# Kernel optimization log

Measured on AMD Instinct MI355X. Metric: run time of the kernel, lower is better.

## Reference

```python
import jax, jax.numpy as jnp
from jax import lax
import numpy as np

T = 131072  # trajectory length


def _model_matrices():
    # F: constant-velocity model on augmented state [pose_t; pose_{t-1}]
    I6 = jnp.eye(6, dtype=jnp.float32)
    F = jnp.zeros((12, 12), dtype=jnp.float32)
    F = F.at[:6, :6].set(2.0 * I6)
    F = F.at[:6, 6:].set(-I6)
    F = F.at[6:, :6].set(I6)
    G = jnp.zeros((12, 6), dtype=jnp.float32)
    G = G.at[:6, :6].set(I6)
    return F, G


def setup_inputs() -> dict:
    key = jax.random.key(0)
    k1, = jax.random.split(key, 1)
    pose_measurements = jax.random.normal(k1, (T, 6), dtype=jnp.float32)
    # SPD noise covariances (scaled identities, as typical in the repo's config)
    process_noise_cov = 0.01 * jnp.eye(6, dtype=jnp.float32)
    measure_noise_cov = 0.05 * jnp.eye(6, dtype=jnp.float32)
    cov_init = jnp.eye(12, dtype=jnp.float32)  # _covariance_matrix_pred buffer
    return {
        "pose_measurements": pose_measurements,
        "process_noise_cov": process_noise_cov,
        "measure_noise_cov": measure_noise_cov,
        "cov_init": cov_init,
    }


def reference(pose_measurements, process_noise_cov, measure_noise_cov, cov_init):
    F, G = _model_matrices()
    Q_aug = G @ process_noise_cov @ G.T  # [[Q, 0], [0, 0]]  (12,12)
    I12 = jnp.eye(12, dtype=jnp.float32)
    z6 = jnp.zeros((12, 6), dtype=jnp.float32)

    def step(carry, meas):
        est, P = carry  # est: (12,), P: (12,12)
        # _predict
        v = est[:6] - est[6:]
        pred = jnp.concatenate([est[:6] + v, est[:6]])  # (12,)
        Pp = F @ P @ F.T + Q_aug
        # _update
        S = Pp[:6, :6] + measure_noise_cov            # (6,6)
        K = Pp[:, :6] @ jnp.linalg.inv(S)             # (12,6)
        est_new = pred + K @ (meas - pred[:6])        # (12,)
        KH = jnp.concatenate([K, z6], axis=1)         # (12,12)
        P_new = (I12 - KH) @ Pp
        return (est_new, P_new), (pred, est_new)

    # rows 0,1 initialized from measurements
    row0 = jnp.concatenate([pose_measurements[0], jnp.zeros(6, dtype=jnp.float32)])
    row1 = jnp.concatenate([pose_measurements[1], pose_measurements[0]])

    (_, _), (preds, ests) = lax.scan(step, (row1, cov_init), pose_measurements[2:])

    head = jnp.stack([row0, row1])                   # (2,12)
    pose_estimate = jnp.concatenate([head, ests], axis=0)    # (T,12)
    pose_prediction = jnp.concatenate([head, preds], axis=0)  # (T,12)
    velocity_estimate = pose_estimate[1:-1, :6] - pose_estimate[1:-1, 6:]

    return (pose_estimate[:, :6], pose_prediction[:, :6], velocity_estimate)
```

## Files before the change

### kernel.cpp

```cpp
#include <hip/hip_runtime.h>

#define T_LEN   131072
#define NSTEPS  (T_LEN - 2)
#define CHUNK   16
#define NCHUNK  8192
#define NCJ     (NCHUNK * 6)
#define CAP     512
#define CPB     64
#define NBLK    (NCHUNK / CPB)
#define K2T     (CPB * 6)

#define OFF_STEADY 16
#define OFF_K1     32
#define OFF_K2     (OFF_K1 + CAP * 4)
#define OFF_LP     (OFF_K2 + CAP * 4)
#define OFF_BT     (OFF_LP + NCHUNK * 16 * 4)
#define OFF_BI     (OFF_BT + NBLK * 16 * 4)

__device__ __forceinline__ int riccati(const float* pnc, const float* mnc,
                                       const float* cov, float* g1t, float* g2t,
                                       float& k1o, float& k2o) {
    float q = pnc[0], r = mnc[0];
    float a = cov[0], b = cov[6], c = cov[6 * 12 + 6];
    float pk1 = -1e30f, pk2 = -1e30f, k1 = 0.f, k2 = 0.f;
    int stable = 0, s;
    for (s = 0; s < CAP; ++s) {
        float bp = 2.0f * a - b;
        float t2 = 2.0f * b - c;
        float ap = 2.0f * bp - t2 + q;
        float cp = a;
        float S  = ap + r;
        float invS = 1.0f / S;
        k1 = ap * invS;
        k2 = bp * invS;
        g1t[s] = k1;
        g2t[s] = k2;
        float om = 1.0f - k1;
        a = om * ap;
        b = om * bp;
        c = cp - k2 * bp;
        if (fabsf(k1 - pk1) <= 5e-7f * fabsf(k1) &&
            fabsf(k2 - pk2) <= 5e-7f * (fabsf(k2) + 1e-20f)) {
            if (++stable >= 8) { ++s; break; }
        } else {
            stable = 0;
        }
        pk1 = k1; pk2 = k2;
    }
    k1o = k1; k2o = k2;
    return s;
}

__global__ __launch_bounds__(K2T) void k_chunk_scan(
    const float* __restrict__ meas, const float* __restrict__ pnc,
    const float* __restrict__ mnc, const float* __restrict__ cov,
    float* __restrict__ ws_f, int* __restrict__ ws_i,
    float* __restrict__ lp, float* __restrict__ btot) {
    __shared__ float g1t[CAP], g2t[CAP];
    __shared__ float lm[CPB][5];
    __shared__ float lu[CPB][13];
    __shared__ int   s_sc;
    __shared__ float s_k1, s_k2;
    int tid = threadIdx.x;
    int cl = tid / 6;
    int j  = tid - 6 * cl;
    int b  = blockIdx.x;
    if (tid == 0) {
        float k1, k2;
        int sc = riccati(pnc, mnc, cov, g1t, g2t, k1, k2);
        s_sc = sc; s_k1 = k1; s_k2 = k2;
    }
    __syncthreads();
    int sc = s_sc;
    float k1s = s_k1, k2s = s_k2;
    if (b == 0) {
        for (int t = tid; t < sc; t += K2T) {
            ws_f[OFF_K1 / 4 + t] = g1t[t];
            ws_f[OFF_K2 / 4 + t] = g2t[t];
        }
        if (tid == 0) {
            ws_i[0] = sc;
            ws_f[OFF_STEADY / 4]     = k1s;
            ws_f[OFF_STEADY / 4 + 1] = k2s;
        }
    }
    int c = b * CPB + cl;
    int s0 = c * CHUNK;
    float m00 = 1.f, m01 = 0.f, m10 = 0.f, m11 = 1.f;
    float u0 = 0.f, u1 = 0.f;
#pragma unroll
    for (int i = 0; i < CHUNK; ++i) {
        int s = s0 + i;
        if (s < NSTEPS) {
            float g1, g2;
            if (b == 0) {
                int si = (s < sc) ? s : 0;
                float ta = g1t[si], tb = g2t[si];
                g1 = (s < sc) ? ta : k1s;
                g2 = (s < sc) ? tb : k2s;
            } else {
                g1 = k1s; g2 = k2s;
            }
            float om  = 1.0f - g1;
            float a00 = 2.0f * om, a01 = -om;
            float a10 = 1.0f - 2.0f * g2, a11 = g2;
            float n00 = a00 * m00 + a01 * m10;
            float n01 = a00 * m01 + a01 * m11;
            float n10 = a10 * m00 + a11 * m10;
            float n11 = a10 * m01 + a11 * m11;
            m00 = n00; m01 = n01; m10 = n10; m11 = n11;
            float mj = meas[(s + 2) * 6 + j];
            float v0 = a00 * u0 + a01 * u1 + g1 * mj;
            float v1 = a10 * u0 + a11 * u1 + g2 * mj;
            u0 = v0; u1 = v1;
        }
    }
    if (j == 0) { lm[cl][0] = m00; lm[cl][1] = m01; lm[cl][2] = m10; lm[cl][3] = m11; }
    lu[cl][j] = u0; lu[cl][6 + j] = u1;
    __syncthreads();
    for (int off = 1; off < CPB; off <<= 1) {
        bool act = (cl >= off);
        float M0, M1, M2, M3, P0, P1, P2, P3, pu0, pu1;
        if (act) {
            M0 = lm[cl][0]; M1 = lm[cl][1]; M2 = lm[cl][2]; M3 = lm[cl][3];
            P0 = lm[cl - off][0]; P1 = lm[cl - off][1];
            P2 = lm[cl - off][2]; P3 = lm[cl - off][3];
            pu0 = lu[cl - off][j]; pu1 = lu[cl - off][6 + j];
        }
        __syncthreads();
        if (act) {
            float nu0 = M0 * pu0 + M1 * pu1 + u0;
            float nu1 = M2 * pu0 + M3 * pu1 + u1;
            u0 = nu0; u1 = nu1;
            lu[cl][j] = u0; lu[cl][6 + j] = u1;
            if (j == 0) {
                lm[cl][0] = M0 * P0 + M1 * P2; lm[cl][1] = M0 * P1 + M1 * P3;
                lm[cl][2] = M2 * P0 + M3 * P2; lm[cl][3] = M2 * P1 + M3 * P3;
            }
        }
        __syncthreads();
    }
    for (int w = tid; w < CPB * 16; w += K2T) {
        int cc = w >> 4, k = w & 15;
        float v = (k < 4) ? lm[cc][k] : lu[cc][k - 4];
        lp[(b * CPB + cc) * 16 + k] = v;
    }
    if (tid < 16) {
        float v = (tid < 4) ? lm[CPB - 1][tid] : lu[CPB - 1][tid - 4];
        btot[b * 16 + tid] = v;
    }
}

__device__ __forceinline__ void compose(const float* L, const float* E, float* D) {
    float n00 = L[0] * E[0] + L[1] * E[2];
    float n01 = L[0] * E[1] + L[1] * E[3];
    float n10 = L[2] * E[0] + L[3] * E[2];
    float n11 = L[2] * E[1] + L[3] * E[3];
#pragma unroll
    for (int j = 0; j < 6; ++j) {
        float e0 = E[4 + j], e1 = E[10 + j];
        D[4 + j]  = L[0] * e0 + L[1] * e1 + L[4 + j];
        D[10 + j] = L[2] * e0 + L[3] * e1 + L[10 + j];
    }
    D[0] = n00; D[1] = n01; D[2] = n10; D[3] = n11;
}

__global__ __launch_bounds__(NBLK) void k_bscan(const float* __restrict__ btot,
                                                float* __restrict__ binc) {
    __shared__ float ld[NBLK * 16];
    int t = threadIdx.x;
    float S[16];
#pragma unroll
    for (int k = 0; k < 16; ++k) { S[k] = btot[t * 16 + k]; ld[t * 16 + k] = S[k]; }
    __syncthreads();
    for (int off = 1; off < NBLK; off <<= 1) {
        bool act = (t >= off);
        float P[16];
        if (act) {
#pragma unroll
            for (int k = 0; k < 16; ++k) P[k] = ld[(t - off) * 16 + k];
        }
        __syncthreads();
        if (act) {
            float D[16];
            compose(S, P, D);
#pragma unroll
            for (int k = 0; k < 16; ++k) { S[k] = D[k]; ld[t * 16 + k] = S[k]; }
        }
        __syncthreads();
    }
#pragma unroll
    for (int k = 0; k < 16; ++k) binc[t * 16 + k] = S[k];
}

__device__ __forceinline__ void load_gains(int s, int sc, const float* k1a,
                                           const float* k2a, float k1s, float k2s,
                                           float& g1, float& g2) {
    int si = (s < sc) ? s : 0;
    float a = k1a[si], b = k2a[si];
    g1 = (s < sc) ? a : k1s;
    g2 = (s < sc) ? b : k2s;
}

__global__ __launch_bounds__(256) void k_emit(
    const float* __restrict__ meas, const float* __restrict__ ws_f,
    const int* __restrict__ ws_i, const float* __restrict__ lp,
    const float* __restrict__ binc, float* __restrict__ out) {
    int g = blockIdx.x * 256 + threadIdx.x;
    if (g >= NCJ) return;
    int c = g / 6;
    int j = g - 6 * c;
    int b = c / CPB, cl = c & (CPB - 1);
    float* est  = out;
    float* pred = out + T_LEN * 6;
    float* vel  = out + T_LEN * 12;
    if (c == 0) {
        float m0 = meas[j], m1 = meas[6 + j];
        est[j] = m0; est[6 + j] = m1;
        pred[j] = m0; pred[6 + j] = m1;
        vel[j] = m1 - m0;
    }
    float zx = meas[6 + j], zy = meas[j];
    if (b > 0) {
        const float* B = binc + (b - 1) * 16;
        float nx = B[0] * zx + B[1] * zy + B[4 + j];
        float ny = B[2] * zx + B[3] * zy + B[10 + j];
        zx = nx; zy = ny;
    }
    if (cl > 0) {
        const float* L = lp + (c - 1) * 16;
        float nx = L[0] * zx + L[1] * zy + L[4 + j];
        float ny = L[2] * zx + L[3] * zy + L[10 + j];
        zx = nx; zy = ny;
    }
    float x = zx, y = zy;
    int sc = ws_i[0];
    float k1s = ws_f[OFF_STEADY / 4], k2s = ws_f[OFF_STEADY / 4 + 1];
    const float* k1a = ws_f + OFF_K1 / 4;
    const float* k2a = ws_f + OFF_K2 / 4;
    int s0 = c * CHUNK;
#pragma unroll
    for (int i = 0; i < CHUNK; ++i) {
        int s = s0 + i;
        if (s < NSTEPS) {
            float g1, g2;
            load_gains(s, sc, k1a, k2a, k1s, k2s, g1, g2);
            float mj  = meas[(s + 2) * 6 + j];
            float vx  = x - y;
            float p   = x + vx;
            float inn = mj - p;
            float xn  = p + g1 * inn;
            float yn  = x + g2 * inn;
            est[(s + 2) * 6 + j]  = xn;
            pred[(s + 2) * 6 + j] = p;
            if (s < NSTEPS - 1) vel[(s + 1) * 6 + j] = xn - yn;
            x = xn; y = yn;
        }
    }
}

extern "C" void kernel_launch(void* const* d_in, const int* in_sizes, int n_in,
                              void* d_out, int out_size, void* d_ws, size_t ws_size,
                              hipStream_t stream) {
    const float* meas = (const float*)d_in[0];
    const float* pnc  = (const float*)d_in[1];
    const float* mnc  = (const float*)d_in[2];
    const float* cov  = (const float*)d_in[3];
    float* ws_f = (float*)d_ws;
    int*   ws_i = (int*)d_ws;
    float* lp   = ws_f + OFF_LP / 4;
    float* btot = ws_f + OFF_BT / 4;
    float* binc = ws_f + OFF_BI / 4;
    float* out  = (float*)d_out;

    k_chunk_scan<<<NBLK, K2T, 0, stream>>>(meas, pnc, mnc, cov, ws_f, ws_i, lp, btot);
    k_bscan<<<1, NBLK, 0, stream>>>(btot, binc);
    k_emit<<<NCJ / 256, 256, 0, stream>>>(meas, ws_f, ws_i, lp, binc, out);
}
```

Measured before the change: 82.32 us.

## Stage emit outputs through LDS for coalesced global stores

The emit kernel now runs one block per chunk group of 384 threads. Each thread writes its est, pred and velocity values into padded shared memory, and the block then writes them back to global memory contiguously. Before, each thread stored with a stride of 6 floats along its own chunk, so writes were scattered across a wide span. The price is extra LDS traffic, three barriers, and more LDS per block, which can lower occupancy.

```diff
diff --git a/kernel.cpp b/kernel.cpp
--- a/kernel.cpp
+++ b/kernel.cpp
@@ -9,6 +9,8 @@
 #define CPB     64
 #define NBLK    (NCHUNK / CPB)
 #define K2T     (CPB * 6)
+#define BLK_E   (CPB * CHUNK * 6)
+#define LDS_E   (BLK_E + CPB)
 
 #define OFF_STEADY 16
 #define OFF_K1     32
@@ -202,19 +204,21 @@
     g2 = (s < sc) ? b : k2s;
 }
 
-__global__ __launch_bounds__(256) void k_emit(
+__global__ __launch_bounds__(K2T) void k_emit(
     const float* __restrict__ meas, const float* __restrict__ ws_f,
     const int* __restrict__ ws_i, const float* __restrict__ lp,
     const float* __restrict__ binc, float* __restrict__ out) {
-    int g = blockIdx.x * 256 + threadIdx.x;
-    if (g >= NCJ) return;
-    int c = g / 6;
-    int j = g - 6 * c;
-    int b = c / CPB, cl = c & (CPB - 1);
+    __shared__ float eld[LDS_E];
+    __shared__ float pld[LDS_E];
+    int tid = threadIdx.x;
+    int b = blockIdx.x;
+    int cl = tid / 6;
+    int j  = tid - 6 * cl;
+    int c  = b * CPB + cl;
     float* est  = out;
     float* pred = out + T_LEN * 6;
     float* vel  = out + T_LEN * 12;
-    if (c == 0) {
+    if (b == 0 && cl == 0) {
         float m0 = meas[j], m1 = meas[6 + j];
         est[j] = m0; est[6 + j] = m1;
         pred[j] = m0; pred[6 + j] = m1;
@@ -239,6 +243,7 @@
     const float* k1a = ws_f + OFF_K1 / 4;
     const float* k2a = ws_f + OFF_K2 / 4;
     int s0 = c * CHUNK;
+    float v[CHUNK];
 #pragma unroll
     for (int i = 0; i < CHUNK; ++i) {
         int s = s0 + i;
@@ -251,10 +256,41 @@
             float inn = mj - p;
             float xn  = p + g1 * inn;
             float yn  = x + g2 * inn;
-            est[(s + 2) * 6 + j]  = xn;
-            pred[(s + 2) * 6 + j] = p;
-            if (s < NSTEPS - 1) vel[(s + 1) * 6 + j] = xn - yn;
+            int lidx = (cl * CHUNK + i) * 6 + j + cl;
+            eld[lidx] = xn;
+            pld[lidx] = p;
+            v[i] = xn - yn;
             x = xn; y = yn;
+        }
+    }
+    __syncthreads();
+    int base = b * BLK_E;
+    const int T6 = T_LEN * 6;
+#pragma unroll
+    for (int k = 0; k < BLK_E / K2T; ++k) {
+        int e = k * K2T + tid;
+        int a = e + e / 96;
+        int g = base + e + 12;
+        if (g < T6) {
+            est[g]  = eld[a];
+            pred[g] = pld[a];
+        }
+    }
+    __syncthreads();
+#pragma unroll
+    for (int i = 0; i < CHUNK; ++i) {
+        if (s0 + i < NSTEPS) {
+            eld[(cl * CHUNK + i) * 6 + j + cl] = v[i];
+        }
+    }
+    __syncthreads();
+#pragma unroll
+    for (int k = 0; k < BLK_E / K2T; ++k) {
+        int e = k * K2T + tid;
+        int a = e + e / 96;
+        int g = base + e + 6;
+        if (g < NSTEPS * 6) {
+            vel[g] = eld[a];
         }
     }
 }
@@ -275,5 +311,5 @@
 
     k_chunk_scan<<<NBLK, K2T, 0, stream>>>(meas, pnc, mnc, cov, ws_f, ws_i, lp, btot);
     k_bscan<<<1, NBLK, 0, stream>>>(btot, binc);
-    k_emit<<<NCJ / 256, 256, 0, stream>>>(meas, ws_f, ws_i, lp, binc, out);
-}
+    k_emit<<<NBLK, K2T, 0, stream>>>(meas, ws_f, ws_i, lp, binc, out);
+}
```

Result: no change. 82.76 us (+0.5%).
